# Optimization experiments

Hardware: AMD Instinct MI355X
Metric: run time of the kernel (lower is better)

Reference implementation:

```python
import jax, jax.numpy as jnp
import numpy as np


def _gelu(x):
    return jax.nn.gelu(x, approximate=False)


def _conv2d(x, w, b, pad=0, dil=1, groups=1):
    y = jax.lax.conv_general_dilated(
        x, w, (1, 1), [(pad, pad), (pad, pad)], rhs_dilation=(dil, dil),
        dimension_numbers=('NCHW', 'OIHW', 'NCHW'), feature_group_count=groups)
    return y + b[None, :, None, None]


def _ln_last(x, g, b, eps=1e-5):
    m = jnp.mean(x, -1, keepdims=True)
    v = jnp.var(x, -1, keepdims=True)
    return (x - m) * jax.lax.rsqrt(v + eps) * g + b


def _ln2d(x, g, b, eps=1e-5):
    # LayerNorm over channel dim of NCHW
    m = jnp.mean(x, 1, keepdims=True)
    v = jnp.var(x, 1, keepdims=True)
    return (x - m) * jax.lax.rsqrt(v + eps) * g[None, :, None, None] + b[None, :, None, None]


def _bilinear(x, py, px):
    # x: [B,C,H,W]; py,px: [B,H,W] float sample coords; zero outside
    B, C, H, W = x.shape
    y0 = jnp.floor(py)
    x0 = jnp.floor(px)
    wy = py - y0
    wx = px - x0
    xf = x.reshape(B, C, H * W)

    def g(yi, xi):
        valid = ((yi >= 0) & (yi < H) & (xi >= 0) & (xi < W)).astype(x.dtype)
        yc = jnp.clip(yi, 0, H - 1).astype(jnp.int32)
        xc = jnp.clip(xi, 0, W - 1).astype(jnp.int32)
        idx = (yc * W + xc).reshape(B, 1, H * W)
        v = jnp.take_along_axis(xf, idx, axis=2).reshape(B, C, H, W)
        return v * valid[:, None]

    return (g(y0, x0) * ((1 - wy) * (1 - wx))[:, None]
            + g(y0, x0 + 1) * ((1 - wy) * wx)[:, None]
            + g(y0 + 1, x0) * (wy * (1 - wx))[:, None]
            + g(y0 + 1, x0 + 1) * (wy * wx)[:, None])


def _deform_dw(x, ow, ob, w, b, dil):
    # modulated deformable depthwise 3x3 conv, offset_groups=1
    B, C, H, W = x.shape
    pad = dil
    off = _conv2d(x, ow, ob, pad=pad, dil=dil)          # [B,27,H,W]
    ox, oy, m = jnp.split(off, 3, axis=1)               # each [B,9,H,W]
    m = jax.nn.sigmoid(m)
    ys = jnp.arange(H, dtype=x.dtype)[None, :, None]
    xs = jnp.arange(W, dtype=x.dtype)[None, None, :]
    acc = jnp.zeros_like(x)
    for ki in range(3):
        for kj in range(3):
            kk = ki * 3 + kj
            py = ys - pad + ki * dil + oy[:, kk]
            px = xs - pad + kj * dil + ox[:, kk]
            s = _bilinear(x, py, px)                    # [B,C,H,W]
            acc = acc + s * m[:, kk][:, None] * w[:, 0, ki, kj][None, :, None, None]
    return acc + b[None, :, None, None]


def _forward(image_embed, inter_prototypes, intra_prototypes, masks,
             proj_w, proj_b, lin_w, lin_b, tok_g, tok_b, alpha,
             in_w, in_b, off0_w, off0_b, dw0_w, dw0_b,
             off1_w, off1_b, dw1_w, dw1_b, cv_w, cv_b, ln_g, ln_b,
             op0_w, op0_b, op1_w, op1_b, op2_w, op2_b,
             out0_w, out0_b, out1_w, out1_b):
    C = image_embed.shape[1]
    scale = C ** -0.5
    # prototype tokens [B,Q,C]
    pt = jnp.einsum('bqc,bnc->bqn', inter_prototypes, intra_prototypes)
    t = jnp.concatenate([inter_prototypes, pt], axis=-1) @ proj_w + proj_b
    t = _gelu(t) @ lin_w + lin_b
    t = _ln_last(t, tok_g, tok_b)
    # mask gating of image features
    pe = jnp.einsum('bnc,bnhw->bchw', intra_prototypes, masks)
    img = image_embed * pe + image_embed
    # DeformAttn
    x = _gelu(_conv2d(img, in_w, in_b))
    a = _deform_dw(x, off0_w, off0_b, dw0_w, dw0_b, dil=1)
    a = _deform_dw(a, off1_w, off1_b, dw1_w, dw1_b, dil=3)
    a = _conv2d(a, cv_w, cv_b)
    x = x * a + img
    x = _ln2d(x, ln_g, ln_b)
    y = _conv2d(x, op0_w, op0_b)
    y = _gelu(_conv2d(y, op1_w, op1_b, pad=1, groups=C))
    y = _conv2d(y, op2_w, op2_b)
    dense = y + x
    # prototype cross-attention over 8 tokens
    attn = jnp.einsum('bchw,bqc->bqhw', dense, t) * scale
    attn = jax.nn.softmax(attn, axis=1)
    attn = jnp.einsum('bqhw,bqc->bchw', attn, t)
    attn = attn + dense * alpha[None, :, None, None]
    o = _gelu(_conv2d(attn, out0_w, out0_b))
    o = _conv2d(o, out1_w, out1_b)
    return o


def setup_inputs():
    key = jax.random.key(0)
    ks = jax.random.split(key, 40)
    B, C, H, W, Q, N = 16, 256, 64, 64, 8, 9
    f32 = jnp.float32

    def rn(k, shp, s=1.0):
        return jax.random.normal(k, shp, f32) * s

    inp = {
        'image_embed': rn(ks[0], (B, C, H, W)),
        'inter_prototypes': rn(ks[1], (B, Q, C)),
        'intra_prototypes': rn(ks[2], (B, N, C)),
        'masks': jax.random.uniform(ks[3], (B, N, H, W), f32),
        'proj_w': rn(ks[4], (C + N, C), 0.02), 'proj_b': jnp.zeros((C,), f32),
        'lin_w': rn(ks[5], (C, C), 0.02), 'lin_b': jnp.zeros((C,), f32),
        'tok_g': 1.0 + rn(ks[6], (C,), 0.05), 'tok_b': rn(ks[7], (C,), 0.05),
        'alpha': jnp.ones((C,), f32) * 0.001,
        'in_w': rn(ks[8], (C, C, 1, 1), 0.02), 'in_b': jnp.zeros((C,), f32),
        'off0_w': rn(ks[9], (27, C, 3, 3), 0.01), 'off0_b': rn(ks[10], (27,), 0.01),
        'dw0_w': rn(ks[11], (C, 1, 3, 3), 0.2), 'dw0_b': jnp.zeros((C,), f32),
        'off1_w': rn(ks[12], (27, C, 3, 3), 0.01), 'off1_b': rn(ks[13], (27,), 0.01),
        'dw1_w': rn(ks[14], (C, 1, 3, 3), 0.2), 'dw1_b': jnp.zeros((C,), f32),
        'cv_w': rn(ks[15], (C, C, 1, 1), 0.02), 'cv_b': jnp.zeros((C,), f32),
        'ln_g': 1.0 + rn(ks[16], (C,), 0.05), 'ln_b': rn(ks[17], (C,), 0.05),
        'op0_w': rn(ks[18], (C, C, 1, 1), 0.02), 'op0_b': jnp.zeros((C,), f32),
        'op1_w': rn(ks[19], (C, 1, 3, 3), 0.2), 'op1_b': jnp.zeros((C,), f32),
        'op2_w': rn(ks[20], (C, C, 1, 1), 0.02), 'op2_b': jnp.zeros((C,), f32),
        'out0_w': rn(ks[21], (C // 2, C, 1, 1), 0.02), 'out0_b': jnp.zeros((C // 2,), f32),
        'out1_w': rn(ks[22], (C, C // 2, 1, 1), 0.02), 'out1_b': jnp.zeros((C,), f32),
    }
    return inp


def reference(image_embed, inter_prototypes, intra_prototypes, masks,
              proj_w, proj_b, lin_w, lin_b, tok_g, tok_b, alpha,
              in_w, in_b, off0_w, off0_b, dw0_w, dw0_b,
              off1_w, off1_b, dw1_w, dw1_b, cv_w, cv_b, ln_g, ln_b,
              op0_w, op0_b, op1_w, op1_b, op2_w, op2_b,
              out0_w, out0_b, out1_w, out1_b):
    return _forward(image_embed, inter_prototypes, intra_prototypes, masks,
                    proj_w, proj_b, lin_w, lin_b, tok_g, tok_b, alpha,
                    in_w, in_b, off0_w, off0_b, dw0_w, dw0_b,
                    off1_w, off1_b, dw1_w, dw1_b, cv_w, cv_b, ln_g, ln_b,
                    op0_w, op0_b, op1_w, op1_b, op2_w, op2_b,
                    out0_w, out0_b, out1_w, out1_b)
```

## Files before the change

kernel.cpp:

```cpp
#include <hip/hip_runtime.h>
#include <math.h>

#define BB 16
#define CC 256
#define HH 64
#define WW 64
#define HWs 4096
#define PP 65536
#define QQ 8
#define NN 9

typedef _Float16 half8_t __attribute__((ext_vector_type(8)));
typedef _Float16 half4_t __attribute__((ext_vector_type(4)));
typedef float floatx4 __attribute__((ext_vector_type(4)));

__device__ __forceinline__ float gelu_f(float x) {
    return 0.5f * x * (1.0f + erff(x * 0.70710678118654752f));
}

__global__ void prep_weights_kernel(const float* __restrict__ off0_w, const float* __restrict__ off1_w,
                                    const float* __restrict__ dw0_w, const float* __restrict__ dw1_w,
                                    const float* __restrict__ op1_w,
                                    const float* __restrict__ in_w, const float* __restrict__ cv_w,
                                    const float* __restrict__ op0_w, const float* __restrict__ op2_w,
                                    const float* __restrict__ out0_w, const float* __restrict__ out1_w,
                                    float* __restrict__ dwt0, float* __restrict__ dwt1,
                                    float* __restrict__ op1t,
                                    _Float16* __restrict__ wh_in, _Float16* __restrict__ wh_cv,
                                    _Float16* __restrict__ wh_op0, _Float16* __restrict__ wh_op2,
                                    _Float16* __restrict__ wh_out0, _Float16* __restrict__ wh_out1,
                                    _Float16* __restrict__ whoff0, _Float16* __restrict__ whoff1) {
    int i = blockIdx.x * 256 + threadIdx.x;
    if (i < 9*256) {
        int c = i & 255;
        int tap = i >> 8;
        dwt0[i] = dw0_w[c*9 + tap];
        dwt1[i] = dw1_w[c*9 + tap];
        op1t[i] = op1_w[c*9 + tap];
    }
    if (i < 65536) {
        wh_in[i]  = (_Float16)in_w[i];
        wh_cv[i]  = (_Float16)cv_w[i];
        wh_op0[i] = (_Float16)op0_w[i];
        wh_op2[i] = (_Float16)op2_w[i];
    }
    if (i < 32768) {
        wh_out0[i] = (_Float16)out0_w[i];
        wh_out1[i] = (_Float16)out1_w[i];
    }
    if (i < 9*32*256) {
        int ci = i & 255;
        int k32 = (i >> 8) & 31;
        int tap = i >> 13;
        float v0 = 0.f, v1 = 0.f;
        if (k32 < 27) {
            v0 = off0_w[(k32*256 + ci)*9 + tap];
            v1 = off1_w[(k32*256 + ci)*9 + tap];
        }
        whoff0[i] = (_Float16)v0;
        whoff1[i] = (_Float16)v1;
    }
}

__global__ void token_kernel(const float* __restrict__ inter, const float* __restrict__ intra,
                             const float* __restrict__ proj_w, const float* __restrict__ proj_b,
                             const float* __restrict__ lin_w, const float* __restrict__ lin_b,
                             const float* __restrict__ tok_g, const float* __restrict__ tok_b,
                             float* __restrict__ t_out) {
    int bq = blockIdx.x;
    int b = bq >> 3, q = bq & 7;
    int c = threadIdx.x;
    __shared__ float inter_s[256];
    __shared__ float pt_s[9];
    __shared__ float g_s[256];
    __shared__ float red[256];
    __shared__ float stat[2];
    inter_s[c] = inter[(b*QQ + q)*CC + c];
    __syncthreads();
    for (int n = 0; n < 9; n++) {
        red[c] = inter_s[c] * intra[(b*NN + n)*CC + c];
        __syncthreads();
        for (int s = 128; s > 0; s >>= 1) {
            if (c < s) red[c] += red[c + s];
            __syncthreads();
        }
        if (c == 0) pt_s[n] = red[0];
        __syncthreads();
    }
    float u = proj_b[c];
    for (int k = 0; k < 256; k++) u += inter_s[k] * proj_w[k*CC + c];
    for (int n = 0; n < 9; n++) u += pt_s[n] * proj_w[(256 + n)*CC + c];
    g_s[c] = gelu_f(u);
    __syncthreads();
    float v = lin_b[c];
    for (int k = 0; k < 256; k++) v += g_s[k] * lin_w[k*CC + c];
    red[c] = v;
    __syncthreads();
    for (int s = 128; s > 0; s >>= 1) { if (c < s) red[c] += red[c + s]; __syncthreads(); }
    if (c == 0) stat[0] = red[0] * (1.0f/256.0f);
    __syncthreads();
    float m = stat[0];
    red[c] = (v - m)*(v - m);
    __syncthreads();
    for (int s = 128; s > 0; s >>= 1) { if (c < s) red[c] += red[c + s]; __syncthreads(); }
    if (c == 0) stat[1] = red[0] * (1.0f/256.0f);
    __syncthreads();
    float var = stat[1];
    float r = rsqrtf(var + 1e-5f);
    t_out[(b*QQ + q)*CC + c] = (v - m) * r * tok_g[c] + tok_b[c];
}

__global__ void img_pe_kernel(const float* __restrict__ ie, const float* __restrict__ intra,
                              const float* __restrict__ masks, float* __restrict__ img) {
    int b = blockIdx.z;
    int c0 = blockIdx.y * 32;
    int s0 = blockIdx.x * 32;
    __shared__ float tile[32][33];
    __shared__ float intra_s[9][32];
    __shared__ float mask_s[9][32];
    int tx = threadIdx.x, ty = threadIdx.y;
    int t = ty*32 + tx;
    for (int i = t; i < 288; i += 256) {
        int n = i >> 5, j = i & 31;
        intra_s[n][j] = intra[(b*NN + n)*CC + c0 + j];
        mask_s[n][j]  = masks[(b*NN + n)*HWs + s0 + j];
    }
    __syncthreads();
    #pragma unroll
    for (int r = 0; r < 4; r++) {
        int cl = ty + 8*r;
        float val = ie[(b*CC + c0 + cl)*HWs + s0 + tx];
        float pe = 0.f;
        #pragma unroll
        for (int n = 0; n < 9; n++) pe += intra_s[n][cl] * mask_s[n][tx];
        tile[cl][tx] = val * (1.0f + pe);
    }
    __syncthreads();
    #pragma unroll
    for (int r = 0; r < 4; r++) {
        int sl = ty + 8*r;
        img[(b*HWs + s0 + sl)*CC + c0 + tx] = tile[tx][sl];
    }
}

template<int CI, int CO, int ACT, int RES, bool INH, int OUT>
__global__ void __launch_bounds__(256) conv1x1_mfma(const void* __restrict__ in, const _Float16* __restrict__ Wh,
        const float* __restrict__ bias, const void* __restrict__ res, float* __restrict__ out,
        _Float16* __restrict__ outh) {
    constexpr int KS = CI/32;
    constexpr int NF = CO/64;
    constexpr int LDR = CI + 8;
    __shared__ __align__(16) _Float16 a_lds[64*LDR];
    int t = threadIdx.x;
    int wid = t >> 6, lane = t & 63;
    int quad = lane >> 4, l16 = lane & 15;
    int p0 = blockIdx.x * 64;
    if (INH) {
        const half8_t* inh = (const half8_t*)in + (size_t)p0*(CI/8);
        for (int i = t; i < 64*(CI/8); i += 256) {
            int r = i/(CI/8), c8 = i%(CI/8);
            *(half8_t*)&a_lds[r*LDR + c8*8] = inh[i];
        }
    } else {
        const float4* inf = (const float4*)in + (size_t)p0*(CI/4);
        for (int i = t; i < 64*(CI/4); i += 256) {
            float4 v = inf[i];
            half4_t hv; hv[0]=(_Float16)v.x; hv[1]=(_Float16)v.y; hv[2]=(_Float16)v.z; hv[3]=(_Float16)v.w;
            int r = i/(CI/4), c4 = i%(CI/4);
            *(half4_t*)&a_lds[r*LDR + c4*4] = hv;
        }
    }
    __syncthreads();
    int n0 = wid*(CO/4);
    floatx4 acc[4][NF];
    #pragma unroll
    for (int mf = 0; mf < 4; mf++)
        #pragma unroll
        for (int nf = 0; nf < NF; nf++)
            #pragma unroll
            for (int r = 0; r < 4; r++) acc[mf][nf][r] = 0.f;
    for (int ks = 0; ks < KS; ks++) {
        int k = ks*32 + quad*8;
        half8_t a[4];
        #pragma unroll
        for (int mf = 0; mf < 4; mf++)
            a[mf] = *(const half8_t*)&a_lds[(mf*16 + l16)*LDR + k];
        half8_t bfr[NF];
        #pragma unroll
        for (int nf = 0; nf < NF; nf++)
            bfr[nf] = *(const half8_t*)&Wh[(size_t)(n0 + nf*16 + l16)*CI + k];
        #pragma unroll
        for (int mf = 0; mf < 4; mf++)
            #pragma unroll
            for (int nf = 0; nf < NF; nf++)
                acc[mf][nf] = __builtin_amdgcn_mfma_f32_16x16x32_f16(a[mf], bfr[nf], acc[mf][nf], 0, 0, 0);
    }
    size_t bb = (size_t)(p0 >> 12) * ((size_t)CO * HWs) + (size_t)(p0 & 4095);
    #pragma unroll
    for (int nf = 0; nf < NF; nf++) {
        int co = n0 + nf*16 + l16;
        float bs = bias[co];
        #pragma unroll
        for (int mf = 0; mf < 4; mf++) {
            #pragma unroll
            for (int r = 0; r < 4; r++) {
                int p = p0 + mf*16 + quad*4 + r;
                float v = acc[mf][nf][r] + bs;
                if (ACT) v = gelu_f(v);
                if (RES == 1) v += ((const float*)res)[(size_t)p*CO + co];
                if (RES == 2) v += (float)((const _Float16*)res)[(size_t)p*CO + co];
                if (OUT == 0 || OUT == 2) out[(size_t)p*CO + co] = v;
                if (OUT == 1 || OUT == 2) outh[(size_t)p*CO + co] = (_Float16)v;
                if (OUT == 3) out[bb + (size_t)co*HWs + (mf*16 + quad*4 + r)] = v;
            }
        }
    }
}

template<int DIL>
__global__ void __launch_bounds__(256) off_conv_mfma(const _Float16* __restrict__ x, const _Float16* __restrict__ Wh,
        const float* __restrict__ bias, float* __restrict__ off) {
    constexpr int LDR = 264;
    __shared__ __align__(16) _Float16 xs[70*LDR];
    int raw = blockIdx.x;
    int bh = (raw & 7) * 128 + (raw >> 3);
    int b = bh >> 6, h = bh & 63;
    int t = threadIdx.x;
    int wid = t >> 6, lane = t & 63;
    int quad = lane >> 4, l16 = lane & 15;
    for (int i = t; i < 6*LDR; i += 256) {
        int r = i/LDR, c = i%LDR;
        int row = (r < 3) ? r : (64 + r);
        xs[row*LDR + c] = (_Float16)0.f;
    }
    floatx4 acc[2];
    #pragma unroll
    for (int nf = 0; nf < 2; nf++)
        #pragma unroll
        for (int r = 0; r < 4; r++) acc[nf][r] = 0.f;
    for (int ki = 0; ki < 3; ki++) {
        int hrow = h + (ki - 1)*DIL;
        __syncthreads();
        if (hrow >= 0 && hrow < 64) {
            const half8_t* row = (const half8_t*)(x + ((size_t)(b*64 + hrow)*64) * 256);
            for (int i = t; i < 2048; i += 256) {
                int r = i >> 5, c8 = i & 31;
                *(half8_t*)&xs[(r + 3)*LDR + c8*8] = row[r*32 + c8];
            }
        } else {
            half8_t z = (half8_t)((_Float16)0.f);
            for (int i = t; i < 2048; i += 256) {
                int r = i >> 5, c8 = i & 31;
                *(half8_t*)&xs[(r + 3)*LDR + c8*8] = z;
            }
        }
        __syncthreads();
        #pragma unroll
        for (int kj = 0; kj < 3; kj++) {
            const _Float16* wt = Wh + (size_t)(ki*3 + kj)*32*256;
            int wrow = wid*16 + l16 + (kj - 1)*DIL + 3;
            #pragma unroll
            for (int cs = 0; cs < 8; cs++) {
                int k = cs*32 + quad*8;
                half8_t a = *(const half8_t*)&xs[wrow*LDR + k];
                half8_t b0 = *(const half8_t*)&wt[(size_t)l16*256 + k];
                half8_t b1 = *(const half8_t*)&wt[(size_t)(16 + l16)*256 + k];
                acc[0] = __builtin_amdgcn_mfma_f32_16x16x32_f16(a, b0, acc[0], 0, 0, 0);
                acc[1] = __builtin_amdgcn_mfma_f32_16x16x32_f16(a, b1, acc[1], 0, 0, 0);
            }
        }
    }
    int pbase = (b*64 + h)*64;
    #pragma unroll
    for (int nf = 0; nf < 2; nf++) {
        int kcol = nf*16 + l16;
        if (kcol < 27) {
            float bs = bias[kcol];
            #pragma unroll
            for (int r = 0; r < 4; r++) {
                int w = wid*16 + quad*4 + r;
                off[(size_t)(pbase + w)*27 + kcol] = acc[nf][r] + bs;
            }
        }
    }
}

template<int DIL>
__global__ void __launch_bounds__(256, 3) deform_kernel(const _Float16* __restrict__ src, const float* __restrict__ off,
        const float* __restrict__ dwt, const float* __restrict__ dwb, _Float16* __restrict__ out) {
    int raw = blockIdx.x;
    int swz = (raw & 7) * 256 + (raw >> 3);
    int whalf = swz & 1;
    int bh = swz >> 1;
    int b = bh >> 6, h = bh & 63;
    int t = threadIdx.x;
    int c4 = t & 63;
    int ps = t >> 6;

    __shared__ float4 wq4[288];
    __shared__ int4   iq4[288];
    __shared__ float  dw_lds[9*256];

    for (int i = t; i < 9*256; i += 256) dw_lds[i] = dwt[i];

    for (int j = t; j < 288; j += 256) {
        int lw = j / 9;
        int kk = j - lw*9;
        int w = whalf*32 + lw;
        int p = (b*64 + h)*64 + w;
        const float* op = off + (size_t)p*27;
        float ox = op[kk];
        float oy = op[9 + kk];
        float mm = op[18 + kk];
        mm = 1.0f / (1.0f + expf(-mm));
        int ki = kk / 3, kj = kk - ki*3;
        float py = (float)(h - DIL + ki*DIL) + oy;
        float px = (float)(w - DIL + kj*DIL) + ox;
        float y0f = floorf(py), x0f = floorf(px);
        float wy = py - y0f, wx = px - x0f;
        int y0 = (int)y0f, x0 = (int)x0f;
        int y1 = y0 + 1, x1 = x0 + 1;
        float w00 = (1.f - wy)*(1.f - wx)*mm;
        float w01 = (1.f - wy)*wx*mm;
        float w10 = wy*(1.f - wx)*mm;
        float w11 = wy*wx*mm;
        bool yv0 = (y0 >= 0) && (y0 < 64);
        bool yv1 = (y1 >= 0) && (y1 < 64);
        bool xv0 = (x0 >= 0) && (x0 < 64);
        bool xv1 = (x1 >= 0) && (x1 < 64);
        int y0c = min(max(y0, 0), 63), y1c = min(max(y1, 0), 63);
        int x0c = min(max(x0, 0), 63), x1c = min(max(x1, 0), 63);
        int base = b*4096;
        float4 wv;
        wv.x = (yv0 && xv0) ? w00 : 0.f;
        wv.y = (yv0 && xv1) ? w01 : 0.f;
        wv.z = (yv1 && xv0) ? w10 : 0.f;
        wv.w = (yv1 && xv1) ? w11 : 0.f;
        wq4[j] = wv;
        int4 iv;
        iv.x = (base + y0c*64 + x0c) << 9;
        iv.y = (base + y0c*64 + x1c) << 9;
        iv.z = (base + y1c*64 + x0c) << 9;
        iv.w = (base + y1c*64 + x1c) << 9;
        iq4[j] = iv;
    }
    __syncthreads();

    float4 bv = ((const float4*)dwb)[c4];
    const char* srcb = (const char*)src + (size_t)c4*8;
    for (int i = 0; i < 8; i++) {
        int lw = ps*8 + i;
        int jb = lw*9;
        int w = whalf*32 + lw;
        int p = (b*64 + h)*64 + w;
        half4_t v[9][4];
        #pragma unroll
        for (int kk = 0; kk < 9; kk++) {
            int4 iv = iq4[jb + kk];
            int o0 = __builtin_amdgcn_readfirstlane(iv.x);
            int o1 = __builtin_amdgcn_readfirstlane(iv.y);
            int o2 = __builtin_amdgcn_readfirstlane(iv.z);
            int o3 = __builtin_amdgcn_readfirstlane(iv.w);
            v[kk][0] = *(const half4_t*)(srcb + o0);
            v[kk][1] = *(const half4_t*)(srcb + o1);
            v[kk][2] = *(const half4_t*)(srcb + o2);
            v[kk][3] = *(const half4_t*)(srcb + o3);
        }
        float4 acc = make_float4(0.f,0.f,0.f,0.f);
        #pragma unroll
        for (int kk = 0; kk < 9; kk++) {
            float4 wv = wq4[jb + kk];
            float4 dw = ((const float4*)dw_lds)[kk*64 + c4];
            float sx = (float)v[kk][0][0]*wv.x + (float)v[kk][1][0]*wv.y + (float)v[kk][2][0]*wv.z + (float)v[kk][3][0]*wv.w;
            float sy = (float)v[kk][0][1]*wv.x + (float)v[kk][1][1]*wv.y + (float)v[kk][2][1]*wv.z + (float)v[kk][3][1]*wv.w;
            float sz = (float)v[kk][0][2]*wv.x + (float)v[kk][1][2]*wv.y + (float)v[kk][2][2]*wv.z + (float)v[kk][3][2]*wv.w;
            float sw = (float)v[kk][0][3]*wv.x + (float)v[kk][1][3]*wv.y + (float)v[kk][2][3]*wv.z + (float)v[kk][3][3]*wv.w;
            acc.x += sx * dw.x;
            acc.y += sy * dw.y;
            acc.z += sz * dw.z;
            acc.w += sw * dw.w;
        }
        half4_t o4;
        o4[0] = (_Float16)(acc.x + bv.x);
        o4[1] = (_Float16)(acc.y + bv.y);
        o4[2] = (_Float16)(acc.z + bv.z);
        o4[3] = (_Float16)(acc.w + bv.w);
        ((half4_t*)out)[(size_t)p*64 + c4] = o4;
    }
}

__global__ void __launch_bounds__(256) gate_ln_kernel(const _Float16* __restrict__ x, const _Float16* __restrict__ a,
        const float* __restrict__ img, const float* __restrict__ g, const float* __restrict__ bb,
        _Float16* __restrict__ out) {
    int t = threadIdx.x;
    int lane = t & 63;
    int wv = t >> 6;
    int p = blockIdx.x*4 + wv;
    half4_t xh = ((const half4_t*)x)[p*64 + lane];
    half4_t ah = ((const half4_t*)a)[p*64 + lane];
    float4 iv = ((const float4*)img)[p*64 + lane];
    float4 v;
    v.x = (float)xh[0]*(float)ah[0] + iv.x;
    v.y = (float)xh[1]*(float)ah[1] + iv.y;
    v.z = (float)xh[2]*(float)ah[2] + iv.z;
    v.w = (float)xh[3]*(float)ah[3] + iv.w;
    float s = v.x + v.y + v.z + v.w;
    float s2 = v.x*v.x + v.y*v.y + v.z*v.z + v.w*v.w;
    #pragma unroll
    for (int o = 1; o < 64; o <<= 1) { s += __shfl_xor(s, o); s2 += __shfl_xor(s2, o); }
    float m = s * (1.f/256.f);
    float var = s2 * (1.f/256.f) - m*m;
    float r = rsqrtf(var + 1e-5f);
    float4 gv = ((const float4*)g)[lane];
    float4 bv = ((const float4*)bb)[lane];
    half4_t o4;
    o4[0] = (_Float16)((v.x - m)*r*gv.x + bv.x);
    o4[1] = (_Float16)((v.y - m)*r*gv.y + bv.y);
    o4[2] = (_Float16)((v.z - m)*r*gv.z + bv.z);
    o4[3] = (_Float16)((v.w - m)*r*gv.w + bv.w);
    ((half4_t*)out)[p*64 + lane] = o4;
}

__global__ void __launch_bounds__(256) dw3x3_kernel(const _Float16* __restrict__ in, const float* __restrict__ wt,
        const float* __restrict__ bias, _Float16* __restrict__ out) {
    int raw = blockIdx.x;
    int swz = (raw & 7) * 2048 + (raw >> 3);
    int gid = swz*256 + threadIdx.x;
    int c4 = gid & 63;
    int p = gid >> 6;
    int w = p & 63;
    int h = (p >> 6) & 63;
    int b = p >> 12;
    float4 acc = ((const float4*)bias)[c4];
    #pragma unroll
    for (int ki = 0; ki < 3; ki++) {
        int hh = h + ki - 1;
        if (hh < 0 || hh >= 64) continue;
        #pragma unroll
        for (int kj = 0; kj < 3; kj++) {
            int wwp = w + kj - 1;
            if (wwp < 0 || wwp >= 64) continue;
            half4_t v = ((const half4_t*)in)[((b*64 + hh)*64 + wwp)*64 + c4];
            float4 wv = ((const float4*)wt)[(ki*3 + kj)*64 + c4];
            acc.x += (float)v[0]*wv.x; acc.y += (float)v[1]*wv.y;
            acc.z += (float)v[2]*wv.z; acc.w += (float)v[3]*wv.w;
        }
    }
    half4_t o4;
    o4[0] = (_Float16)gelu_f(acc.x);
    o4[1] = (_Float16)gelu_f(acc.y);
    o4[2] = (_Float16)gelu_f(acc.z);
    o4[3] = (_Float16)gelu_f(acc.w);
    ((half4_t*)out)[p*64 + c4] = o4;
}

__global__ void __launch_bounds__(256) attn_mfma_kernel(const _Float16* __restrict__ dense,
        const float* __restrict__ tok, const float* __restrict__ alpha, _Float16* __restrict__ out) {
    __shared__ __align__(16) _Float16 d_lds[64*264];
    __shared__ __align__(16) _Float16 t_q[16*264];
    __shared__ __align__(16) _Float16 t_t[258*24];
    __shared__ __align__(16) _Float16 w_lds[64*40];
    __shared__ float al_s[256];
    int t = threadIdx.x;
    int wid = t >> 6, lane = t & 63;
    int quad = lane >> 4, l16 = lane & 15;
    int p0 = blockIdx.x * 64;
    int b = p0 >> 12;

    for (int i = t; i < 16*264; i += 256) t_q[i] = (_Float16)0.f;
    for (int i = t; i < 258*24; i += 256) t_t[i] = (_Float16)0.f;
    for (int i = t; i < 64*40;  i += 256) w_lds[i] = (_Float16)0.f;
    __syncthreads();

    const half8_t* dh = (const half8_t*)dense + (size_t)p0*32;
    for (int i = t; i < 2048; i += 256) {
        int r = i >> 5, c8 = i & 31;
        *(half8_t*)&d_lds[r*264 + c8*8] = dh[i];
    }
    for (int i = t; i < 512; i += 256) {
        int q = i >> 6, j = i & 63;
        float4 tv = ((const float4*)tok)[(b*8 + q)*64 + j];
        int c0 = j*4;
        t_q[q*264 + c0 + 0] = (_Float16)tv.x;
        t_q[q*264 + c0 + 1] = (_Float16)tv.y;
        t_q[q*264 + c0 + 2] = (_Float16)tv.z;
        t_q[q*264 + c0 + 3] = (_Float16)tv.w;
        t_t[(c0 + 0)*24 + q] = (_Float16)tv.x;
        t_t[(c0 + 1)*24 + q] = (_Float16)tv.y;
        t_t[(c0 + 2)*24 + q] = (_Float16)tv.z;
        t_t[(c0 + 3)*24 + q] = (_Float16)tv.w;
    }
    al_s[t] = alpha[t];
    __syncthreads();

    floatx4 s4;
    s4[0]=0.f; s4[1]=0.f; s4[2]=0.f; s4[3]=0.f;
    #pragma unroll
    for (int ks = 0; ks < 8; ks++) {
        int k = ks*32 + quad*8;
        half8_t a = *(const half8_t*)&d_lds[(wid*16 + l16)*264 + k];
        half8_t bf = *(const half8_t*)&t_q[l16*264 + k];
        s4 = __builtin_amdgcn_mfma_f32_16x16x32_f16(a, bf, s4, 0, 0, 0);
    }
    float wgt[4];
    #pragma unroll
    for (int r = 0; r < 4; r++) {
        float sc = s4[r] * 0.0625f;
        float mx = sc;
        mx = fmaxf(mx, __shfl_xor(mx, 1));
        mx = fmaxf(mx, __shfl_xor(mx, 2));
        mx = fmaxf(mx, __shfl_xor(mx, 4));
        float e = expf(sc - mx);
        float dn = e;
        dn += __shfl_xor(dn, 1);
        dn += __shfl_xor(dn, 2);
        dn += __shfl_xor(dn, 4);
        wgt[r] = e / dn;
    }
    if (l16 < 8) {
        #pragma unroll
        for (int r = 0; r < 4; r++)
            w_lds[(wid*16 + quad*4 + r)*40 + l16] = (_Float16)wgt[r];
    }
    __syncthreads();

    half8_t aw = *(const half8_t*)&w_lds[(wid*16 + l16)*40 + quad*8];
    floatx4 z4; z4[0]=0.f; z4[1]=0.f; z4[2]=0.f; z4[3]=0.f;
    floatx4 acc[16];
    #pragma unroll
    for (int nf = 0; nf < 16; nf++) {
        half8_t bf = *(const half8_t*)&t_t[(nf*16 + l16)*24 + quad*8];
        acc[nf] = __builtin_amdgcn_mfma_f32_16x16x32_f16(aw, bf, z4, 0, 0, 0);
    }
    #pragma unroll
    for (int nf = 0; nf < 16; nf++) {
        int co = nf*16 + l16;
        float al = al_s[co];
        #pragma unroll
        for (int r = 0; r < 4; r++) {
            int px = wid*16 + quad*4 + r;
            float d = (float)d_lds[px*264 + co];
            float o = acc[nf][r] + d*al;
            out[(size_t)(p0 + px)*256 + co] = (_Float16)o;
        }
    }
}

extern "C" void kernel_launch(void* const* d_in, const int* in_sizes, int n_in,
                              void* d_out, int out_size, void* d_ws, size_t ws_size,
                              hipStream_t stream) {
    const float* image_embed = (const float*)d_in[0];
    const float* inter_p     = (const float*)d_in[1];
    const float* intra_p     = (const float*)d_in[2];
    const float* masks       = (const float*)d_in[3];
    const float* proj_w      = (const float*)d_in[4];
    const float* proj_b      = (const float*)d_in[5];
    const float* lin_w       = (const float*)d_in[6];
    const float* lin_b       = (const float*)d_in[7];
    const float* tok_g       = (const float*)d_in[8];
    const float* tok_b       = (const float*)d_in[9];
    const float* alpha       = (const float*)d_in[10];
    const float* in_w        = (const float*)d_in[11];
    const float* in_b        = (const float*)d_in[12];
    const float* off0_w      = (const float*)d_in[13];
    const float* off0_b      = (const float*)d_in[14];
    const float* dw0_w       = (const float*)d_in[15];
    const float* dw0_b       = (const float*)d_in[16];
    const float* off1_w      = (const float*)d_in[17];
    const float* off1_b      = (const float*)d_in[18];
    const float* dw1_w       = (const float*)d_in[19];
    const float* dw1_b       = (const float*)d_in[20];
    const float* cv_w        = (const float*)d_in[21];
    const float* cv_b        = (const float*)d_in[22];
    const float* ln_g        = (const float*)d_in[23];
    const float* ln_b        = (const float*)d_in[24];
    const float* op0_w       = (const float*)d_in[25];
    const float* op0_b       = (const float*)d_in[26];
    const float* op1_w       = (const float*)d_in[27];
    const float* op1_b       = (const float*)d_in[28];
    const float* op2_w       = (const float*)d_in[29];
    const float* op2_b       = (const float*)d_in[30];
    const float* out0_w      = (const float*)d_in[31];
    const float* out0_b      = (const float*)d_in[32];
    const float* out1_w      = (const float*)d_in[33];
    const float* out1_b      = (const float*)d_in[34];
    (void)ws_size; (void)in_sizes; (void)n_in; (void)out_size;

    float* ws = (float*)d_ws;
    const size_t BIG = (size_t)PP * CC;
    float* A   = ws;
    float* Bb  = A + BIG;
    float* Cb  = Bb + BIG;
    float* OFF = Cb + BIG;
    float* TOK = OFF + (size_t)PP*27;
    float* DWT0 = TOK + BB*QQ*CC;
    float* DWT1 = DWT0 + 9*256;
    float* OP1T = DWT1 + 9*256;
    _Float16* WH_IN   = (_Float16*)(OP1T + 9*256);
    _Float16* WH_CV   = WH_IN + 65536;
    _Float16* WH_OP0  = WH_CV + 65536;
    _Float16* WH_OP2  = WH_OP0 + 65536;
    _Float16* WH_OUT0 = WH_OP2 + 65536;
    _Float16* WH_OUT1 = WH_OUT0 + 32768;
    _Float16* WHOFF0  = WH_OUT1 + 32768;
    _Float16* WHOFF1  = WHOFF0 + 9*32*256;
    _Float16* XH   = (_Float16*)Bb;
    _Float16* A1H  = XH + (size_t)PP*CC;
    _Float16* A2H  = (_Float16*)Cb;
    _Float16* AH   = A2H + (size_t)PP*CC;
    _Float16* XLNH = (_Float16*)d_out;
    _Float16* Y0H  = (_Float16*)A;
    _Float16* Y1H  = Y0H + (size_t)PP*CC;
    _Float16* DENH = (_Float16*)Cb;
    _Float16* ATH  = (_Float16*)Bb;
    _Float16* O0H  = (_Float16*)Cb + (size_t)PP*CC;

    prep_weights_kernel<<<(9*32*256 + 255)/256, 256, 0, stream>>>(
        off0_w, off1_w, dw0_w, dw1_w, op1_w,
        in_w, cv_w, op0_w, op2_w, out0_w, out1_w,
        DWT0, DWT1, OP1T,
        WH_IN, WH_CV, WH_OP0, WH_OP2, WH_OUT0, WH_OUT1, WHOFF0, WHOFF1);
    token_kernel<<<BB*QQ, 256, 0, stream>>>(inter_p, intra_p, proj_w, proj_b,
                                            lin_w, lin_b, tok_g, tok_b, TOK);
    img_pe_kernel<<<dim3(HWs/32, CC/32, BB), dim3(32,8), 0, stream>>>(image_embed, intra_p, masks, A);
    conv1x1_mfma<256,256,1,0,false,1><<<PP/64, 256, 0, stream>>>(A, WH_IN, in_b, nullptr, nullptr, XH);
    off_conv_mfma<1><<<BB*HH, 256, 0, stream>>>(XH, WHOFF0, off0_b, OFF);
    deform_kernel<1><<<BB*HH*2, 256, 0, stream>>>(XH, OFF, DWT0, dw0_b, A1H);
    off_conv_mfma<3><<<BB*HH, 256, 0, stream>>>(A1H, WHOFF1, off1_b, OFF);
    deform_kernel<3><<<BB*HH*2, 256, 0, stream>>>(A1H, OFF, DWT1, dw1_b, A2H);
    conv1x1_mfma<256,256,0,0,true,1><<<PP/64, 256, 0, stream>>>(A2H, WH_CV, cv_b, nullptr, nullptr, AH);
    gate_ln_kernel<<<PP/4, 256, 0, stream>>>(XH, AH, A, ln_g, ln_b, XLNH);
    conv1x1_mfma<256,256,0,0,true,1><<<PP/64, 256, 0, stream>>>(XLNH, WH_OP0, op0_b, nullptr, nullptr, Y0H);
    dw3x3_kernel<<<PP*64/256, 256, 0, stream>>>(Y0H, OP1T, op1_b, Y1H);
    conv1x1_mfma<256,256,0,2,true,1><<<PP/64, 256, 0, stream>>>(Y1H, WH_OP2, op2_b, XLNH, nullptr, DENH);
    attn_mfma_kernel<<<PP/64, 256, 0, stream>>>(DENH, TOK, alpha, ATH);
    conv1x1_mfma<256,128,1,0,true,1><<<PP/64, 256, 0, stream>>>(ATH, WH_OUT0, out0_b, nullptr, nullptr, O0H);
    conv1x1_mfma<128,256,0,0,true,3><<<PP/64, 256, 0, stream>>>(O0H, WH_OUT1, out1_b, nullptr, (float*)d_out, nullptr);
}
```

Before: 813.4 us.

## Fuse cv conv with gated LayerNorm, store image as fp16, vectorize conv stores

Fuses the cv 1x1 conv with the gate-multiply, residual and channel LayerNorm into a single MFMA kernel that uses cross-wave reductions. This removes a kernel launch and the fp32/fp16 round trip of the intermediate activation. The img_pe output is now stored as fp16, which halves that traffic and lets the first conv take fp16 input. The conv epilogue remaps output channels per lane so fp16 stores are vectorized, and the NCHW output is written as float4. Deform drops its occupancy hint and gains a sched barrier; the main risk is the extra fp16 rounding of the residual image.

```diff
diff --git a/kernel.cpp b/kernel.cpp
--- a/kernel.cpp
+++ b/kernel.cpp
@@ -12,6 +12,7 @@
 
 typedef _Float16 half8_t __attribute__((ext_vector_type(8)));
 typedef _Float16 half4_t __attribute__((ext_vector_type(4)));
+typedef _Float16 half2_t __attribute__((ext_vector_type(2)));
 typedef float floatx4 __attribute__((ext_vector_type(4)));
 
 __device__ __forceinline__ float gelu_f(float x) {
@@ -111,7 +112,7 @@
 }
 
 __global__ void img_pe_kernel(const float* __restrict__ ie, const float* __restrict__ intra,
-                              const float* __restrict__ masks, float* __restrict__ img) {
+                              const float* __restrict__ masks, _Float16* __restrict__ img) {
     int b = blockIdx.z;
     int c0 = blockIdx.y * 32;
     int s0 = blockIdx.x * 32;
@@ -139,13 +140,13 @@
     #pragma unroll
     for (int r = 0; r < 4; r++) {
         int sl = ty + 8*r;
-        img[(b*HWs + s0 + sl)*CC + c0 + tx] = tile[tx][sl];
-    }
-}
-
-template<int CI, int CO, int ACT, int RES, bool INH, int OUT>
-__global__ void __launch_bounds__(256) conv1x1_mfma(const void* __restrict__ in, const _Float16* __restrict__ Wh,
-        const float* __restrict__ bias, const void* __restrict__ res, float* __restrict__ out,
+        img[(b*HWs + s0 + sl)*CC + c0 + tx] = (_Float16)tile[tx][sl];
+    }
+}
+
+template<int CI, int CO, int ACT, int RES, int OUT>
+__global__ void __launch_bounds__(256) conv1x1_mfma(const _Float16* __restrict__ in, const _Float16* __restrict__ Wh,
+        const float* __restrict__ bias, const _Float16* __restrict__ res, float* __restrict__ out,
         _Float16* __restrict__ outh) {
     constexpr int KS = CI/32;
     constexpr int NF = CO/64;
@@ -155,20 +156,12 @@
     int wid = t >> 6, lane = t & 63;
     int quad = lane >> 4, l16 = lane & 15;
     int p0 = blockIdx.x * 64;
-    if (INH) {
+    {
         const half8_t* inh = (const half8_t*)in + (size_t)p0*(CI/8);
         for (int i = t; i < 64*(CI/8); i += 256) {
             int r = i/(CI/8), c8 = i%(CI/8);
             *(half8_t*)&a_lds[r*LDR + c8*8] = inh[i];
         }
-    } else {
-        const float4* inf = (const float4*)in + (size_t)p0*(CI/4);
-        for (int i = t; i < 64*(CI/4); i += 256) {
-            float4 v = inf[i];
-            half4_t hv; hv[0]=(_Float16)v.x; hv[1]=(_Float16)v.y; hv[2]=(_Float16)v.z; hv[3]=(_Float16)v.w;
-            int r = i/(CI/4), c4 = i%(CI/4);
-            *(half4_t*)&a_lds[r*LDR + c4*4] = hv;
-        }
     }
     __syncthreads();
     int n0 = wid*(CO/4);
@@ -187,32 +180,162 @@
             a[mf] = *(const half8_t*)&a_lds[(mf*16 + l16)*LDR + k];
         half8_t bfr[NF];
         #pragma unroll
-        for (int nf = 0; nf < NF; nf++)
-            bfr[nf] = *(const half8_t*)&Wh[(size_t)(n0 + nf*16 + l16)*CI + k];
+        for (int nf = 0; nf < NF; nf++) {
+            int brow = (OUT == 1) ? (n0 + l16*NF + nf) : (n0 + nf*16 + l16);
+            bfr[nf] = *(const half8_t*)&Wh[(size_t)brow*CI + k];
+        }
         #pragma unroll
         for (int mf = 0; mf < 4; mf++)
             #pragma unroll
             for (int nf = 0; nf < NF; nf++)
                 acc[mf][nf] = __builtin_amdgcn_mfma_f32_16x16x32_f16(a[mf], bfr[nf], acc[mf][nf], 0, 0, 0);
     }
-    size_t bb = (size_t)(p0 >> 12) * ((size_t)CO * HWs) + (size_t)(p0 & 4095);
-    #pragma unroll
-    for (int nf = 0; nf < NF; nf++) {
-        int co = n0 + nf*16 + l16;
-        float bs = bias[co];
+    if (OUT == 1) {
+        int cb = n0 + l16*NF;
+        float bs[NF];
+        #pragma unroll
+        for (int j = 0; j < NF; j++) bs[j] = bias[cb + j];
         #pragma unroll
         for (int mf = 0; mf < 4; mf++) {
             #pragma unroll
             for (int r = 0; r < 4; r++) {
                 int p = p0 + mf*16 + quad*4 + r;
-                float v = acc[mf][nf][r] + bs;
-                if (ACT) v = gelu_f(v);
-                if (RES == 1) v += ((const float*)res)[(size_t)p*CO + co];
-                if (RES == 2) v += (float)((const _Float16*)res)[(size_t)p*CO + co];
-                if (OUT == 0 || OUT == 2) out[(size_t)p*CO + co] = v;
-                if (OUT == 1 || OUT == 2) outh[(size_t)p*CO + co] = (_Float16)v;
-                if (OUT == 3) out[bb + (size_t)co*HWs + (mf*16 + quad*4 + r)] = v;
+                half4_t rh;
+                if (RES == 2 && NF == 4) rh = *(const half4_t*)&res[(size_t)p*CO + cb];
+                _Float16 tmp[NF];
+                #pragma unroll
+                for (int j = 0; j < NF; j++) {
+                    float v = acc[mf][j][r] + bs[j];
+                    if (ACT) v = gelu_f(v);
+                    if (RES == 2 && NF == 4) v += (float)rh[j];
+                    tmp[j] = (_Float16)v;
+                }
+                if (NF == 4) {
+                    half4_t o4; o4[0]=tmp[0]; o4[1]=tmp[1]; o4[2]=tmp[2]; o4[3]=tmp[3];
+                    *(half4_t*)&outh[(size_t)p*CO + cb] = o4;
+                } else {
+                    half2_t o2; o2[0]=tmp[0]; o2[1]=tmp[1];
+                    *(half2_t*)&outh[(size_t)p*CO + cb] = o2;
+                }
             }
+        }
+    } else {
+        size_t bb = (size_t)(p0 >> 12) * ((size_t)CO * HWs) + (size_t)(p0 & 4095);
+        #pragma unroll
+        for (int nf = 0; nf < NF; nf++) {
+            int co = n0 + nf*16 + l16;
+            float bs = bias[co];
+            #pragma unroll
+            for (int mf = 0; mf < 4; mf++) {
+                float4 vst;
+                vst.x = acc[mf][nf][0] + bs;
+                vst.y = acc[mf][nf][1] + bs;
+                vst.z = acc[mf][nf][2] + bs;
+                vst.w = acc[mf][nf][3] + bs;
+                if (ACT) { vst.x=gelu_f(vst.x); vst.y=gelu_f(vst.y); vst.z=gelu_f(vst.z); vst.w=gelu_f(vst.w); }
+                *(float4*)&out[bb + (size_t)co*HWs + mf*16 + quad*4] = vst;
+            }
+        }
+    }
+}
+
+__global__ void __launch_bounds__(256) conv_cv_ln_kernel(const _Float16* __restrict__ in, const _Float16* __restrict__ Wh,
+        const float* __restrict__ bias, const _Float16* __restrict__ X, const _Float16* __restrict__ IMG,
+        const float* __restrict__ g, const float* __restrict__ bb2, _Float16* __restrict__ out) {
+    constexpr int CI = 256, KS = 8, NF = 4, LDR = 264;
+    __shared__ __align__(16) _Float16 a_lds[64*LDR];
+    __shared__ float rs[64][4];
+    __shared__ float rs2[64][4];
+    __shared__ float st[64][2];
+    int t = threadIdx.x;
+    int wid = t >> 6, lane = t & 63;
+    int quad = lane >> 4, l16 = lane & 15;
+    int p0 = blockIdx.x * 64;
+    {
+        const half8_t* inh = (const half8_t*)in + (size_t)p0*32;
+        for (int i = t; i < 2048; i += 256) {
+            int r = i >> 5, c8 = i & 31;
+            *(half8_t*)&a_lds[r*LDR + c8*8] = inh[i];
+        }
+    }
+    __syncthreads();
+    int n0 = wid*64;
+    floatx4 acc[4][4];
+    #pragma unroll
+    for (int mf = 0; mf < 4; mf++)
+        #pragma unroll
+        for (int nf = 0; nf < 4; nf++)
+            #pragma unroll
+            for (int r = 0; r < 4; r++) acc[mf][nf][r] = 0.f;
+    for (int ks = 0; ks < KS; ks++) {
+        int k = ks*32 + quad*8;
+        half8_t a[4];
+        #pragma unroll
+        for (int mf = 0; mf < 4; mf++)
+            a[mf] = *(const half8_t*)&a_lds[(mf*16 + l16)*LDR + k];
+        half8_t bfr[4];
+        #pragma unroll
+        for (int nf = 0; nf < 4; nf++)
+            bfr[nf] = *(const half8_t*)&Wh[(size_t)(n0 + l16*4 + nf)*CI + k];
+        #pragma unroll
+        for (int mf = 0; mf < 4; mf++)
+            #pragma unroll
+            for (int nf = 0; nf < 4; nf++)
+                acc[mf][nf] = __builtin_amdgcn_mfma_f32_16x16x32_f16(a[mf], bfr[nf], acc[mf][nf], 0, 0, 0);
+    }
+    int cb = n0 + l16*4;
+    float bs[4];
+    #pragma unroll
+    for (int j = 0; j < 4; j++) bs[j] = bias[cb + j];
+    #pragma unroll
+    for (int mf = 0; mf < 4; mf++) {
+        #pragma unroll
+        for (int r = 0; r < 4; r++) {
+            int px_l = mf*16 + quad*4 + r;
+            size_t off = (size_t)(p0 + px_l)*256 + cb;
+            half4_t xh = *(const half4_t*)&X[off];
+            half4_t ih = *(const half4_t*)&IMG[off];
+            float s = 0.f, s2 = 0.f;
+            #pragma unroll
+            for (int j = 0; j < 4; j++) {
+                float v = acc[mf][j][r] + bs[j];
+                v = (float)xh[j]*v + (float)ih[j];
+                acc[mf][j][r] = v;
+                s += v; s2 += v*v;
+            }
+            s += __shfl_xor(s, 1); s2 += __shfl_xor(s2, 1);
+            s += __shfl_xor(s, 2); s2 += __shfl_xor(s2, 2);
+            s += __shfl_xor(s, 4); s2 += __shfl_xor(s2, 4);
+            s += __shfl_xor(s, 8); s2 += __shfl_xor(s2, 8);
+            if (l16 == 0) { rs[px_l][wid] = s; rs2[px_l][wid] = s2; }
+        }
+    }
+    __syncthreads();
+    if (t < 64) {
+        float m = 0.f, q = 0.f;
+        #pragma unroll
+        for (int w = 0; w < 4; w++) { m += rs[t][w]; q += rs2[t][w]; }
+        m *= (1.0f/256.0f);
+        float var = q*(1.0f/256.0f) - m*m;
+        st[t][0] = m;
+        st[t][1] = rsqrtf(var + 1e-5f);
+    }
+    __syncthreads();
+    float ga[4], ba[4];
+    #pragma unroll
+    for (int j = 0; j < 4; j++) { ga[j] = g[cb + j]; ba[j] = bb2[cb + j]; }
+    #pragma unroll
+    for (int mf = 0; mf < 4; mf++) {
+        #pragma unroll
+        for (int r = 0; r < 4; r++) {
+            int px_l = mf*16 + quad*4 + r;
+            float m = st[px_l][0];
+            float ri = st[px_l][1];
+            half4_t o4;
+            #pragma unroll
+            for (int j = 0; j < 4; j++)
+                o4[j] = (_Float16)((acc[mf][j][r] - m)*ri*ga[j] + ba[j]);
+            *(half4_t*)&out[(size_t)(p0 + px_l)*256 + cb] = o4;
         }
     }
 }
@@ -286,7 +409,7 @@
 }
 
 template<int DIL>
-__global__ void __launch_bounds__(256, 3) deform_kernel(const _Float16* __restrict__ src, const float* __restrict__ off,
+__global__ void __launch_bounds__(256) deform_kernel(const _Float16* __restrict__ src, const float* __restrict__ off,
         const float* __restrict__ dwt, const float* __restrict__ dwb, _Float16* __restrict__ out) {
     int raw = blockIdx.x;
     int swz = (raw & 7) * 256 + (raw >> 3);
@@ -366,6 +489,7 @@
             v[kk][2] = *(const half4_t*)(srcb + o2);
             v[kk][3] = *(const half4_t*)(srcb + o3);
         }
+        __builtin_amdgcn_sched_barrier(0);
         float4 acc = make_float4(0.f,0.f,0.f,0.f);
         #pragma unroll
         for (int kk = 0; kk < 9; kk++) {
@@ -387,38 +511,6 @@
         o4[3] = (_Float16)(acc.w + bv.w);
         ((half4_t*)out)[(size_t)p*64 + c4] = o4;
     }
-}
-
-__global__ void __launch_bounds__(256) gate_ln_kernel(const _Float16* __restrict__ x, const _Float16* __restrict__ a,
-        const float* __restrict__ img, const float* __restrict__ g, const float* __restrict__ bb,
-        _Float16* __restrict__ out) {
-    int t = threadIdx.x;
-    int lane = t & 63;
-    int wv = t >> 6;
-    int p = blockIdx.x*4 + wv;
-    half4_t xh = ((const half4_t*)x)[p*64 + lane];
-    half4_t ah = ((const half4_t*)a)[p*64 + lane];
-    float4 iv = ((const float4*)img)[p*64 + lane];
-    float4 v;
-    v.x = (float)xh[0]*(float)ah[0] + iv.x;
-    v.y = (float)xh[1]*(float)ah[1] + iv.y;
-    v.z = (float)xh[2]*(float)ah[2] + iv.z;
-    v.w = (float)xh[3]*(float)ah[3] + iv.w;
-    float s = v.x + v.y + v.z + v.w;
-    float s2 = v.x*v.x + v.y*v.y + v.z*v.z + v.w*v.w;
-    #pragma unroll
-    for (int o = 1; o < 64; o <<= 1) { s += __shfl_xor(s, o); s2 += __shfl_xor(s2, o); }
-    float m = s * (1.f/256.f);
-    float var = s2 * (1.f/256.f) - m*m;
-    float r = rsqrtf(var + 1e-5f);
-    float4 gv = ((const float4*)g)[lane];
-    float4 bv = ((const float4*)bb)[lane];
-    half4_t o4;
-    o4[0] = (_Float16)((v.x - m)*r*gv.x + bv.x);
-    o4[1] = (_Float16)((v.y - m)*r*gv.y + bv.y);
-    o4[2] = (_Float16)((v.z - m)*r*gv.z + bv.z);
-    o4[3] = (_Float16)((v.w - m)*r*gv.w + bv.w);
-    ((half4_t*)out)[p*64 + lane] = o4;
 }
 
 __global__ void __launch_bounds__(256) dw3x3_kernel(const _Float16* __restrict__ in, const float* __restrict__ wt,
@@ -604,16 +696,16 @@
     _Float16* WH_OUT1 = WH_OUT0 + 32768;
     _Float16* WHOFF0  = WH_OUT1 + 32768;
     _Float16* WHOFF1  = WHOFF0 + 9*32*256;
+    _Float16* IMGH = (_Float16*)A;
+    _Float16* Y0H  = (_Float16*)A;
+    _Float16* Y1H  = Y0H + (size_t)PP*CC;
     _Float16* XH   = (_Float16*)Bb;
     _Float16* A1H  = XH + (size_t)PP*CC;
+    _Float16* ATH  = (_Float16*)Bb;
     _Float16* A2H  = (_Float16*)Cb;
-    _Float16* AH   = A2H + (size_t)PP*CC;
+    _Float16* DENH = (_Float16*)Cb;
+    _Float16* O0H  = (_Float16*)Cb + (size_t)PP*CC;
     _Float16* XLNH = (_Float16*)d_out;
-    _Float16* Y0H  = (_Float16*)A;
-    _Float16* Y1H  = Y0H + (size_t)PP*CC;
-    _Float16* DENH = (_Float16*)Cb;
-    _Float16* ATH  = (_Float16*)Bb;
-    _Float16* O0H  = (_Float16*)Cb + (size_t)PP*CC;
 
     prep_weights_kernel<<<(9*32*256 + 255)/256, 256, 0, stream>>>(
         off0_w, off1_w, dw0_w, dw1_w, op1_w,
@@ -622,18 +714,17 @@
         WH_IN, WH_CV, WH_OP0, WH_OP2, WH_OUT0, WH_OUT1, WHOFF0, WHOFF1);
     token_kernel<<<BB*QQ, 256, 0, stream>>>(inter_p, intra_p, proj_w, proj_b,
                                             lin_w, lin_b, tok_g, tok_b, TOK);
-    img_pe_kernel<<<dim3(HWs/32, CC/32, BB), dim3(32,8), 0, stream>>>(image_embed, intra_p, masks, A);
-    conv1x1_mfma<256,256,1,0,false,1><<<PP/64, 256, 0, stream>>>(A, WH_IN, in_b, nullptr, nullptr, XH);
+    img_pe_kernel<<<dim3(HWs/32, CC/32, BB), dim3(32,8), 0, stream>>>(image_embed, intra_p, masks, IMGH);
+    conv1x1_mfma<256,256,1,0,1><<<PP/64, 256, 0, stream>>>(IMGH, WH_IN, in_b, nullptr, nullptr, XH);
     off_conv_mfma<1><<<BB*HH, 256, 0, stream>>>(XH, WHOFF0, off0_b, OFF);
     deform_kernel<1><<<BB*HH*2, 256, 0, stream>>>(XH, OFF, DWT0, dw0_b, A1H);
     off_conv_mfma<3><<<BB*HH, 256, 0, stream>>>(A1H, WHOFF1, off1_b, OFF);
     deform_kernel<3><<<BB*HH*2, 256, 0, stream>>>(A1H, OFF, DWT1, dw1_b, A2H);
-    conv1x1_mfma<256,256,0,0,true,1><<<PP/64, 256, 0, stream>>>(A2H, WH_CV, cv_b, nullptr, nullptr, AH);
-    gate_ln_kernel<<<PP/4, 256, 0, stream>>>(XH, AH, A, ln_g, ln_b, XLNH);
-    conv1x1_mfma<256,256,0,0,true,1><<<PP/64, 256, 0, stream>>>(XLNH, WH_OP0, op0_b, nullptr, nullptr, Y0H);
+    conv_cv_ln_kernel<<<PP/64, 256, 0, stream>>>(A2H, WH_CV, cv_b, XH, IMGH, ln_g, ln_b, XLNH);
+    conv1x1_mfma<256,256,0,0,1><<<PP/64, 256, 0, stream>>>(XLNH, WH_OP0, op0_b, nullptr, nullptr, Y0H);
     dw3x3_kernel<<<PP*64/256, 256, 0, stream>>>(Y0H, OP1T, op1_b, Y1H);
-    conv1x1_mfma<256,256,0,2,true,1><<<PP/64, 256, 0, stream>>>(Y1H, WH_OP2, op2_b, XLNH, nullptr, DENH);
+    conv1x1_mfma<256,256,0,2,1><<<PP/64, 256, 0, stream>>>(Y1H, WH_OP2, op2_b, XLNH, nullptr, DENH);
     attn_mfma_kernel<<<PP/64, 256, 0, stream>>>(DENH, TOK, alpha, ATH);
-    conv1x1_mfma<256,128,1,0,true,1><<<PP/64, 256, 0, stream>>>(ATH, WH_OUT0, out0_b, nullptr, nullptr, O0H);
-    conv1x1_mfma<128,256,0,0,true,3><<<PP/64, 256, 0, stream>>>(O0H, WH_OUT1, out1_b, nullptr, (float*)d_out, nullptr);
-}
+    conv1x1_mfma<256,128,1,0,1><<<PP/64, 256, 0, stream>>>(ATH, WH_OUT0, out0_b, nullptr, nullptr, O0H);
+    conv1x1_mfma<128,256,0,0,3><<<PP/64, 256, 0, stream>>>(O0H, WH_OUT1, out1_b, nullptr, (float*)d_out, nullptr);
+}
```

Measured after the change: 769.9 us. 1.06x faster.
